# Kernel optimization log

Measured on AMD Instinct MI355X. Metric: run time of the kernel, lower is better.

Reference implementation:

```python
import jax, jax.numpy as jnp
import numpy as np
import math

DIM = 1024
NUM_HEADS = 16
HEAD_DIM = DIM // NUM_HEADS
ROPE_BASE = 10000.0


def _rope_cos_sin(seq_len, head_dim, dtype):
    inv_freq = 1.0 / (ROPE_BASE ** (jnp.arange(0, head_dim, 2, dtype=jnp.float32) / head_dim))
    t = jnp.arange(seq_len, dtype=jnp.float32)
    freqs = jnp.einsum('i,j->ij', t, inv_freq)          # (S, head_dim/2)
    emb = jnp.concatenate([freqs, freqs], axis=-1)      # (S, head_dim)
    return jnp.cos(emb).astype(dtype), jnp.sin(emb).astype(dtype)


def _rotate_half(x):
    x1, x2 = jnp.split(x, 2, axis=-1)
    return jnp.concatenate([-x2, x1], axis=-1)


def setup_inputs() -> dict:
    key = jax.random.key(0)
    kx, kq, kk, kv, ko = jax.random.split(key, 5)
    B, S = 4, 2048
    scale = 1.0 / math.sqrt(DIM)
    x = jax.random.normal(kx, (B, S, DIM), dtype=jnp.float32)
    Wq = jax.random.normal(kq, (DIM, DIM), dtype=jnp.float32) * scale
    Wk = jax.random.normal(kk, (DIM, DIM), dtype=jnp.float32) * scale
    Wv = jax.random.normal(kv, (DIM, DIM), dtype=jnp.float32) * scale
    Wo = jax.random.normal(ko, (DIM, DIM), dtype=jnp.float32) * scale
    mask = jnp.tril(jnp.ones((S, S), dtype=jnp.int32))  # causal mask
    return {"x": x, "Wq": Wq, "Wk": Wk, "Wv": Wv, "Wo": Wo, "mask": mask}


def reference(x, Wq, Wk, Wv, Wo, mask):
    B, S, _ = x.shape
    # projections (nn.Linear: y = x @ W.T)
    def split_heads(t):
        return t.reshape(B, S, NUM_HEADS, HEAD_DIM).transpose(0, 2, 1, 3)  # (B,H,S,D)
    q = split_heads(x @ Wq.T)
    k = split_heads(x @ Wk.T)
    v = split_heads(x @ Wv.T)
    # RoPE
    cos, sin = _rope_cos_sin(S, HEAD_DIM, x.dtype)      # (S, D)
    cos = cos[None, None]; sin = sin[None, None]
    q = q * cos + _rotate_half(q) * sin
    k = k * cos + _rotate_half(k) * sin
    # attention
    scores = jnp.einsum('bhsd,bhtd->bhst', q, k) / math.sqrt(HEAD_DIM)
    neg_inf = jnp.asarray(-jnp.inf, dtype=scores.dtype)
    scores = jnp.where(mask[None, None] == 0, neg_inf, scores)
    attn = jax.nn.softmax(scores, axis=-1)
    out = jnp.einsum('bhst,bhtd->bhsd', attn, v)        # (B,H,S,D)
    out = out.transpose(0, 2, 1, 3).reshape(B, S, DIM)
    return out @ Wo.T
```

## Files before the change

### kernel.cpp

```cpp
#include <hip/hip_runtime.h>
#include <hip/hip_bf16.h>

#define BDIM 1024
#define NH 16
#define HD 64
#define BB 4
#define SS 2048
#define MTOT (BB*SS)
#define NT (SS/64)

typedef __bf16 bf16x8 __attribute__((ext_vector_type(8)));
typedef float f32x4 __attribute__((ext_vector_type(4)));

__device__ __forceinline__ unsigned short f2b(float f){
    __bf16 h = (__bf16)f;
    return __builtin_bit_cast(unsigned short, h);
}

__device__ __forceinline__ unsigned cvtpk(float lo, float hi){
    unsigned u;
    asm("v_cvt_pk_bf16_f32 %0, %1, %2" : "=v"(u) : "v"(lo), "v"(hi));
    return u;
}

__device__ __forceinline__ void ld16(const unsigned short* g, unsigned short* l){
    __builtin_amdgcn_global_load_lds(
        (const __attribute__((address_space(1))) unsigned int*)(const void*)g,
        (__attribute__((address_space(3))) unsigned int*)(void*)l, 16, 0, 0);
}

__global__ void setup_all(const float* __restrict__ x,
                          const float* __restrict__ Wq, const float* __restrict__ Wk,
                          const float* __restrict__ Wv, const float* __restrict__ Wo,
                          unsigned short* __restrict__ xb,
                          unsigned short* __restrict__ oq, unsigned short* __restrict__ ok,
                          unsigned short* __restrict__ ov, unsigned short* __restrict__ oo,
                          float2* __restrict__ rt){
    const int bid = blockIdx.x;
    const int tid = threadIdx.x;
    if (bid < 8192){
        int i = bid * 256 + tid;
        float4 v = ((const float4*)x)[i];
        ushort4 o;
        o.x = f2b(v.x); o.y = f2b(v.y); o.z = f2b(v.z); o.w = f2b(v.w);
        ((ushort4*)xb)[i] = o;
    } else if (bid < 12288){
        int idx = bid - 8192;
        int which = idx >> 10;
        const float* in = (which == 0) ? Wq : (which == 1) ? Wk : (which == 2) ? Wv : Wo;
        unsigned short* out = (which == 0) ? oq : (which == 1) ? ok : (which == 2) ? ov : oo;
        int i = (idx & 1023) * 256 + tid;
        float4 v = ((const float4*)in)[i];
        ushort4 o;
        o.x = f2b(v.x); o.y = f2b(v.y); o.z = f2b(v.z); o.w = f2b(v.w);
        ((ushort4*)out)[i] = o;
    } else {
        int i = (bid - 12288) * 256 + tid;
        int s = i >> 5, d = i & 31;
        float theta = (float)s * exp2f(-0.41524101186092029f * (float)d);
        float sn, c;
        sincosf(theta, &sn, &c);
        rt[i] = make_float2(c, sn);
    }
}

#define TILE_US 4096

__device__ __forceinline__ void swz_xy(int& xs, int& ys){
    int id = blockIdx.x + 8*blockIdx.y;
    xs = id >> 6;
    int t = id & 63;
    ys = (t & 7)*8 + (t >> 3);
}

__device__ __forceinline__ void rope_store(
    const f32x4 acc[4][4], float qs, unsigned short* __restrict__ C,
    const float2* __restrict__ Rt, int m0, int bh, int wr, int lh, int ll)
{
    #pragma unroll
    for (int i = 0; i < 4; ++i)
        #pragma unroll
        for (int r = 0; r < 4; ++r){
            int m = m0 + wr*64 + i*16 + lh*4 + r;
            int s = m & (SS-1);
            int kt = s >> 6;
            const float2* rowcs = Rt + (s << 5);
            size_t fb = ((size_t)(bh*NT + kt)*8 + i)*512 + (size_t)(lh*4 + r)*8;
            #pragma unroll
            for (int jl = 0; jl < 2; ++jl){
                int d_lo = jl*16 + ll;
                float2 cs = rowcs[d_lo];
                float a_lo = acc[i][jl][r], a_hi = acc[i][jl+2][r];
                float y_lo = (a_lo*cs.x - a_hi*cs.y) * qs;
                float y_hi = (a_hi*cs.x + a_lo*cs.y) * qs;
                size_t off = fb + (size_t)(jl*2 + (ll>>3))*128 + (ll&7);
                C[off]        = f2b(y_lo);
                C[off + 2048] = f2b(y_hi);
            }
        }
}

__global__ __launch_bounds__(256, 2) void gemm_qkv(
    const unsigned short* __restrict__ Xb,
    const unsigned short* __restrict__ Wq,
    const unsigned short* __restrict__ Wk,
    const unsigned short* __restrict__ Wv,
    const float2* __restrict__ Rt,
    unsigned short* __restrict__ Qt,
    unsigned short* __restrict__ Kt,
    unsigned short* __restrict__ VTt)
{
    __shared__ alignas(16) unsigned short At [128*64];
    __shared__ alignas(16) unsigned short Bt0[128*64];
    __shared__ alignas(16) unsigned short Bt1[128*64];
    __shared__ alignas(16) unsigned short Bt2[128*64];

    int xs, ys;
    swz_xy(xs, ys);
    const int m0 = ys*128, n0 = xs*128;

    const int tid  = threadIdx.x;
    const int lane = tid & 63;
    const int wave = tid >> 6;
    const int wr = wave >> 1, wc = wave & 1;
    const int lh = lane >> 4, ll = lane & 15;
    const int K = 1024;

    f32x4 accq[4][4] = {}, acck[4][4] = {}, accv[4][4] = {};

    for (int k0 = 0; k0 < K; k0 += 64){
        #pragma unroll
        for (int c = 0; c < 4; ++c){
            int g   = c*256 + tid;
            int row = g >> 3;
            int off = (g & 7) * 8;
            int base = (c*256 + wave*64) * 8;
            ld16(Xb + (size_t)(m0+row)*K + k0 + off, At  + base);
            ld16(Wq + (size_t)(n0+row)*K + k0 + off, Bt0 + base);
            ld16(Wk + (size_t)(n0+row)*K + k0 + off, Bt1 + base);
            ld16(Wv + (size_t)(n0+row)*K + k0 + off, Bt2 + base);
        }
        __syncthreads();
        #pragma unroll
        for (int ks = 0; ks < 2; ++ks){
            bf16x8 af[4];
            #pragma unroll
            for (int i = 0; i < 4; ++i)
                af[i] = *(const bf16x8*)(At + (wr*64 + i*16 + ll)*64 + ks*32 + lh*8);
            {
                bf16x8 b[4];
                #pragma unroll
                for (int j = 0; j < 4; ++j)
                    b[j] = *(const bf16x8*)(Bt0 + (wc*64 + j*16 + ll)*64 + ks*32 + lh*8);
                #pragma unroll
                for (int i = 0; i < 4; ++i)
                    #pragma unroll
                    for (int j = 0; j < 4; ++j)
                        accq[i][j] = __builtin_amdgcn_mfma_f32_16x16x32_bf16(af[i], b[j], accq[i][j], 0, 0, 0);
            }
            {
                bf16x8 b[4];
                #pragma unroll
                for (int j = 0; j < 4; ++j)
                    b[j] = *(const bf16x8*)(Bt1 + (wc*64 + j*16 + ll)*64 + ks*32 + lh*8);
                #pragma unroll
                for (int i = 0; i < 4; ++i)
                    #pragma unroll
                    for (int j = 0; j < 4; ++j)
                        acck[i][j] = __builtin_amdgcn_mfma_f32_16x16x32_bf16(af[i], b[j], acck[i][j], 0, 0, 0);
            }
            {
                bf16x8 b[4];
                #pragma unroll
                for (int j = 0; j < 4; ++j)
                    b[j] = *(const bf16x8*)(Bt2 + (wc*64 + j*16 + ll)*64 + ks*32 + lh*8);
                #pragma unroll
                for (int i = 0; i < 4; ++i)
                    #pragma unroll
                    for (int j = 0; j < 4; ++j)
                        accv[i][j] = __builtin_amdgcn_mfma_f32_16x16x32_bf16(af[i], b[j], accv[i][j], 0, 0, 0);
            }
        }
        __syncthreads();
    }

    const int h  = xs*2 + wc;
    const int b  = m0 >> 11;
    const int bh = b*NH + h;

    rope_store(accq, 0.125f * 1.44269504f, Qt, Rt, m0, bh, wr, lh, ll);
    rope_store(acck, 1.0f,                 Kt, Rt, m0, bh, wr, lh, ll);

    {
        const int s0 = (m0 & (SS-1)) + wr*64;
        const int kt = s0 >> 6;
        #pragma unroll
        for (int i = 0; i < 4; ++i)
            #pragma unroll
            for (int j = 0; j < 4; ++j){
                unsigned short tmp[4];
                #pragma unroll
                for (int r = 0; r < 4; ++r)
                    tmp[r] = f2b(accv[i][j][r]);
                size_t off = ((size_t)(bh*NT + kt)*8 + (i>>1)*4 + j)*512
                           + (size_t)(((i&1)*2 + (lh>>1))*16 + ll)*8 + (lh&1)*4;
                *(uint2*)(VTt + off) = *(const uint2*)tmp;
            }
    }
}

__global__ __launch_bounds__(256, 4) void gemm_out(
    const unsigned short* __restrict__ Ab,
    const unsigned short* __restrict__ Wo,
    float* __restrict__ Cout)
{
    __shared__ alignas(16) unsigned short At[128*64];
    __shared__ alignas(16) unsigned short Bt[128*64];
    int xs, ys;
    swz_xy(xs, ys);
    const int m0 = ys * 128, n0 = xs * 128;

    const int tid  = threadIdx.x;
    const int lane = tid & 63;
    const int wave = tid >> 6;
    const int wr = wave >> 1, wc = wave & 1;
    const int lh = lane >> 4, ll = lane & 15;
    const int K = 1024;

    f32x4 acc[4][4] = {};
    for (int k0 = 0; k0 < K; k0 += 64){
        #pragma unroll
        for (int c = 0; c < 4; ++c){
            int g   = c*256 + tid;
            int row = g >> 3;
            int off = (g & 7) * 8;
            int base = (c*256 + wave*64) * 8;
            ld16(Ab + (size_t)(m0+row)*K + k0 + off, At + base);
            ld16(Wo + (size_t)(n0+row)*K + k0 + off, Bt + base);
        }
        __syncthreads();
        #pragma unroll
        for (int ks = 0; ks < 2; ++ks){
            bf16x8 af[4], bfr[4];
            #pragma unroll
            for (int i = 0; i < 4; ++i)
                af[i] = *(const bf16x8*)(At + (wr*64 + i*16 + ll)*64 + ks*32 + lh*8);
            #pragma unroll
            for (int j = 0; j < 4; ++j)
                bfr[j] = *(const bf16x8*)(Bt + (wc*64 + j*16 + ll)*64 + ks*32 + lh*8);
            #pragma unroll
            for (int i = 0; i < 4; ++i)
                #pragma unroll
                for (int j = 0; j < 4; ++j)
                    acc[i][j] = __builtin_amdgcn_mfma_f32_16x16x32_bf16(af[i], bfr[j], acc[i][j], 0, 0, 0);
        }
        __syncthreads();
    }

    #pragma unroll
    for (int i = 0; i < 4; ++i)
        #pragma unroll
        for (int j = 0; j < 4; ++j)
            #pragma unroll
            for (int r = 0; r < 4; ++r){
                int m = m0 + wr*64 + i*16 + lh*4 + r;
                int n = n0 + wc*64 + j*16 + ll;
                Cout[(size_t)m*BDIM + n] = acc[i][j][r];
            }
}

__device__ __forceinline__ void attn_tile(
    const bf16x8 qf[2], bool diag, int ws, int lane, int lh, int ll,
    const unsigned short* Ksh, const unsigned short* Vsh,
    float& li, f32x4 o[4])
{
    f32x4 sc[4] = {};
    #pragma unroll
    for (int ks = 0; ks < 2; ++ks)
        #pragma unroll
        for (int j = 0; j < 4; ++j){
            bf16x8 kfr = *(const bf16x8*)(Ksh + (ks*4 + j)*512 + lane*8);
            sc[j] = __builtin_amdgcn_mfma_f32_16x16x32_bf16(kfr, qf[ks], sc[j], 0, 0, 0);
        }
    if (diag){
        int qrow = ws*16 + ll;
        #pragma unroll
        for (int j = 0; j < 4; ++j)
            #pragma unroll
            for (int r = 0; r < 4; ++r)
                if (j*16 + lh*4 + r > qrow) sc[j][r] = -1e30f;
    }
    #pragma unroll
    for (int j = 0; j < 4; ++j)
        #pragma unroll
        for (int r = 0; r < 4; ++r)
            sc[j][r] = exp2f(sc[j][r] - 28.0f);
    float s = 0.f;
    #pragma unroll
    for (int j = 0; j < 4; ++j)
        s += (sc[j][0] + sc[j][1]) + (sc[j][2] + sc[j][3]);
    li += s;
    #pragma unroll
    for (int ks = 0; ks < 2; ++ks){
        unsigned a = cvtpk(sc[2*ks][0],   sc[2*ks][1]);
        unsigned b = cvtpk(sc[2*ks+1][0], sc[2*ks+1][1]);
        unsigned c = cvtpk(sc[2*ks][2],   sc[2*ks][3]);
        unsigned d = cvtpk(sc[2*ks+1][2], sc[2*ks+1][3]);
        asm("v_permlane32_swap_b32 %0, %1" : "+v"(a), "+v"(b));
        asm("v_permlane16_swap_b32 %0, %1" : "+v"(a), "+v"(b));
        asm("v_permlane32_swap_b32 %0, %1" : "+v"(c), "+v"(d));
        asm("v_permlane16_swap_b32 %0, %1" : "+v"(c), "+v"(d));
        uint4 uu = make_uint4(a, c, b, d);
        bf16x8 pf = __builtin_bit_cast(bf16x8, uu);
        #pragma unroll
        for (int t = 0; t < 4; ++t){
            bf16x8 vf = *(const bf16x8*)(Vsh + (ks*4 + t)*512 + lane*8);
            o[t] = __builtin_amdgcn_mfma_f32_16x16x32_bf16(pf, vf, o[t], 0, 0, 0);
        }
    }
}

__device__ __forceinline__ void store_o(
    unsigned short* S, const f32x4 o[4], const float li[4],
    int lane, int lh, int ll, int q0w, int b, int h,
    unsigned short* __restrict__ Obuf)
{
    #pragma unroll
    for (int r = 0; r < 4; ++r){
        float inv = 1.0f / li[r];
        #pragma unroll
        for (int t = 0; t < 4; ++t)
            S[(lh*4 + r)*72 + t*16 + ll] = f2b(o[t][r] * inv);
    }
    int row = lane >> 2, c4 = (lane & 3) * 8;
    size_t rb = ((size_t)(b*SS + q0w + row))*BDIM + h*HD;
    *(uint4*)(Obuf + rb + c4)      = *(uint4*)(S + row*72 + c4);
    *(uint4*)(Obuf + rb + 32 + c4) = *(uint4*)(S + row*72 + 32 + c4);
}

__global__ __launch_bounds__(512, 4) void attn_kernel(
    const unsigned short* __restrict__ Qt,
    const unsigned short* __restrict__ Kt,
    const unsigned short* __restrict__ VTt,
    unsigned short* __restrict__ Obuf)
{
    __shared__ alignas(16) unsigned short Ksh[2][TILE_US];
    __shared__ alignas(16) unsigned short Vsh[2][TILE_US];
    __shared__ alignas(16) unsigned short Psh[8][16*72];

    const int tid  = threadIdx.x;
    const int lane = tid & 63;
    const int wave = tid >> 6;
    const int grp  = wave >> 2;
    const int ws   = wave & 3;
    const int lh = lane >> 4, ll = lane & 15;
    const int bx = blockIdx.x;
    const int bh = blockIdx.y;

    const int tS = (grp == 0) ? bx        : 15 - bx;
    const int tL = (grp == 0) ? NT-1 - bx : 16 + bx;
    const int ktMax = NT-1 - bx;

    const unsigned short* Qhf = Qt  + (size_t)bh * NT * TILE_US;
    const unsigned short* Khf = Kt  + (size_t)bh * NT * TILE_US;
    const unsigned short* Vhf = VTt + (size_t)bh * NT * TILE_US;

    bf16x8 qfS[2], qfL[2];
    #pragma unroll
    for (int ks = 0; ks < 2; ++ks){
        qfS[ks] = *(const bf16x8*)(Qhf + (size_t)(tS*8 + ks*4 + ws)*512 + lane*8);
        qfL[ks] = *(const bf16x8*)(Qhf + (size_t)(tL*8 + ks*4 + ws)*512 + lane*8);
    }

    f32x4 oS[4] = {}, oL[4] = {};
    float liS = 0.f, liL = 0.f;

    const int tb = tid * 8;

    {
        uint4 k0 = *(const uint4*)(Khf + tb);
        uint4 v0 = *(const uint4*)(Vhf + tb);
        *(uint4*)(&Ksh[0][0] + tb) = k0;
        *(uint4*)(&Vsh[0][0] + tb) = v0;
    }
    __syncthreads();

    int cur = 0;
    for (int kt = 0; kt <= ktMax; ++kt){
        uint4 kr, vr;
        if (kt < ktMax){
            size_t nb = (size_t)(kt + 1) * TILE_US + tb;
            kr = *(const uint4*)(Khf + nb);
            vr = *(const uint4*)(Vhf + nb);
        }
        if (kt <= tL)
            attn_tile(qfL, kt == tL, ws, lane, lh, ll, &Ksh[cur][0], &Vsh[cur][0], liL, oL);
        if (kt <= tS)
            attn_tile(qfS, kt == tS, ws, lane, lh, ll, &Ksh[cur][0], &Vsh[cur][0], liS, oS);
        if (kt < ktMax){
            *(uint4*)(&Ksh[cur^1][0] + tb) = kr;
            *(uint4*)(&Vsh[cur^1][0] + tb) = vr;
        }
        __syncthreads();
        cur ^= 1;
    }

    liS += __shfl_xor(liS, 16); liS += __shfl_xor(liS, 32);
    liL += __shfl_xor(liL, 16); liL += __shfl_xor(liL, 32);
    float livS[4], livL[4];
    #pragma unroll
    for (int r = 0; r < 4; ++r){
        livS[r] = __shfl(liS, lh*4 + r);
        livL[r] = __shfl(liL, lh*4 + r);
    }

    int b = bh >> 4, h = bh & 15;
    store_o(Psh[wave], oS, livS, lane, lh, ll, tS*64 + ws*16, b, h, Obuf);
    store_o(Psh[wave], oL, livL, lane, lh, ll, tL*64 + ws*16, b, h, Obuf);
}

extern "C" void kernel_launch(void* const* d_in, const int* in_sizes, int n_in,
                              void* d_out, int out_size, void* d_ws, size_t ws_size,
                              hipStream_t stream) {
    const float* x  = (const float*)d_in[0];
    const float* Wq = (const float*)d_in[1];
    const float* Wk = (const float*)d_in[2];
    const float* Wv = (const float*)d_in[3];
    const float* Wo = (const float*)d_in[4];

    char* w = (char*)d_ws;
    unsigned short* xb  = (unsigned short*)(w);
    unsigned short* wqb = (unsigned short*)(w + (16u  << 20));
    unsigned short* wkb = (unsigned short*)(w + (18u  << 20));
    unsigned short* wvb = (unsigned short*)(w + (20u  << 20));
    unsigned short* wob = (unsigned short*)(w + (22u  << 20));
    unsigned short* Qt  = (unsigned short*)(w + (24u  << 20));
    unsigned short* Kt  = (unsigned short*)(w + (40u  << 20));
    unsigned short* VTt = (unsigned short*)(w + (56u  << 20));
    unsigned short* Ob  = (unsigned short*)(w + (72u  << 20));
    float2*         Rt  = (float2*)(w + (88u << 20));

    setup_all<<<12544, 256, 0, stream>>>(x, Wq, Wk, Wv, Wo, xb, wqb, wkb, wvb, wob, Rt);

    gemm_qkv<<<dim3(8, 64), 256, 0, stream>>>(xb, wqb, wkb, wvb, Rt, Qt, Kt, VTt);
    attn_kernel<<<dim3(8, 64), 512, 0, stream>>>(Qt, Kt, VTt, Ob);
    gemm_out<<<dim3(8, 64), 256, 0, stream>>>(Ob, wob, (float*)d_out);
}
```

Before: 292.9 us.

## Shrink QKV GEMM N-tile to one head and remap blocks per XCD

Halves the QKV projection tile width from 128 to 64 columns (one head per block), doubling the grid to 1024 blocks, shrinking shared memory and accumulators, and raising launch bounds to 3 blocks per CU. Each wave now covers 32 rows across all 64 columns, and the RoPE and V-transpose store indexing is updated to match. Block IDs are remapped so that consecutive IDs going to the same XCD share M rows, aiming at better L2 reuse of X. The cost is less operand reuse per block: each block loads the X tile for only half as much output.

```diff
diff --git a/kernel.cpp b/kernel.cpp
--- a/kernel.cpp
+++ b/kernel.cpp
@@ -73,34 +73,7 @@
     ys = (t & 7)*8 + (t >> 3);
 }
 
-__device__ __forceinline__ void rope_store(
-    const f32x4 acc[4][4], float qs, unsigned short* __restrict__ C,
-    const float2* __restrict__ Rt, int m0, int bh, int wr, int lh, int ll)
-{
-    #pragma unroll
-    for (int i = 0; i < 4; ++i)
-        #pragma unroll
-        for (int r = 0; r < 4; ++r){
-            int m = m0 + wr*64 + i*16 + lh*4 + r;
-            int s = m & (SS-1);
-            int kt = s >> 6;
-            const float2* rowcs = Rt + (s << 5);
-            size_t fb = ((size_t)(bh*NT + kt)*8 + i)*512 + (size_t)(lh*4 + r)*8;
-            #pragma unroll
-            for (int jl = 0; jl < 2; ++jl){
-                int d_lo = jl*16 + ll;
-                float2 cs = rowcs[d_lo];
-                float a_lo = acc[i][jl][r], a_hi = acc[i][jl+2][r];
-                float y_lo = (a_lo*cs.x - a_hi*cs.y) * qs;
-                float y_hi = (a_hi*cs.x + a_lo*cs.y) * qs;
-                size_t off = fb + (size_t)(jl*2 + (ll>>3))*128 + (ll&7);
-                C[off]        = f2b(y_lo);
-                C[off + 2048] = f2b(y_hi);
-            }
-        }
-}
-
-__global__ __launch_bounds__(256, 2) void gemm_qkv(
+__global__ __launch_bounds__(256, 3) void gemm_qkv(
     const unsigned short* __restrict__ Xb,
     const unsigned short* __restrict__ Wq,
     const unsigned short* __restrict__ Wk,
@@ -111,22 +84,25 @@
     unsigned short* __restrict__ VTt)
 {
     __shared__ alignas(16) unsigned short At [128*64];
-    __shared__ alignas(16) unsigned short Bt0[128*64];
-    __shared__ alignas(16) unsigned short Bt1[128*64];
-    __shared__ alignas(16) unsigned short Bt2[128*64];
-
-    int xs, ys;
-    swz_xy(xs, ys);
-    const int m0 = ys*128, n0 = xs*128;
+    __shared__ alignas(16) unsigned short Bt0[64*64];
+    __shared__ alignas(16) unsigned short Bt1[64*64];
+    __shared__ alignas(16) unsigned short Bt2[64*64];
+
+    const int id    = blockIdx.x + 16*blockIdx.y;
+    const int xcd   = id & 7;
+    const int chunk = id >> 3;
+    const int xs    = chunk >> 3;
+    const int ys    = xcd*8 + (chunk & 7);
+    const int m0 = ys*128, n0 = xs*64;
 
     const int tid  = threadIdx.x;
     const int lane = tid & 63;
     const int wave = tid >> 6;
-    const int wr = wave >> 1, wc = wave & 1;
+    const int wr   = wave;
     const int lh = lane >> 4, ll = lane & 15;
     const int K = 1024;
 
-    f32x4 accq[4][4] = {}, acck[4][4] = {}, accv[4][4] = {};
+    f32x4 accq[2][4] = {}, acck[2][4] = {}, accv[2][4] = {};
 
     for (int k0 = 0; k0 < K; k0 += 64){
         #pragma unroll
@@ -134,8 +110,14 @@
             int g   = c*256 + tid;
             int row = g >> 3;
             int off = (g & 7) * 8;
+            ld16(Xb + (size_t)(m0+row)*K + k0 + off, At + (c*256 + wave*64)*8);
+        }
+        #pragma unroll
+        for (int c = 0; c < 2; ++c){
+            int g   = c*256 + tid;
+            int row = g >> 3;
+            int off = (g & 7) * 8;
             int base = (c*256 + wave*64) * 8;
-            ld16(Xb + (size_t)(m0+row)*K + k0 + off, At  + base);
             ld16(Wq + (size_t)(n0+row)*K + k0 + off, Bt0 + base);
             ld16(Wk + (size_t)(n0+row)*K + k0 + off, Bt1 + base);
             ld16(Wv + (size_t)(n0+row)*K + k0 + off, Bt2 + base);
@@ -143,17 +125,17 @@
         __syncthreads();
         #pragma unroll
         for (int ks = 0; ks < 2; ++ks){
-            bf16x8 af[4];
-            #pragma unroll
-            for (int i = 0; i < 4; ++i)
-                af[i] = *(const bf16x8*)(At + (wr*64 + i*16 + ll)*64 + ks*32 + lh*8);
+            bf16x8 af[2];
+            #pragma unroll
+            for (int i = 0; i < 2; ++i)
+                af[i] = *(const bf16x8*)(At + (wr*32 + i*16 + ll)*64 + ks*32 + lh*8);
             {
                 bf16x8 b[4];
                 #pragma unroll
                 for (int j = 0; j < 4; ++j)
-                    b[j] = *(const bf16x8*)(Bt0 + (wc*64 + j*16 + ll)*64 + ks*32 + lh*8);
-                #pragma unroll
-                for (int i = 0; i < 4; ++i)
+                    b[j] = *(const bf16x8*)(Bt0 + (j*16 + ll)*64 + ks*32 + lh*8);
+                #pragma unroll
+                for (int i = 0; i < 2; ++i)
                     #pragma unroll
                     for (int j = 0; j < 4; ++j)
                         accq[i][j] = __builtin_amdgcn_mfma_f32_16x16x32_bf16(af[i], b[j], accq[i][j], 0, 0, 0);
@@ -162,9 +144,9 @@
                 bf16x8 b[4];
                 #pragma unroll
                 for (int j = 0; j < 4; ++j)
-                    b[j] = *(const bf16x8*)(Bt1 + (wc*64 + j*16 + ll)*64 + ks*32 + lh*8);
-                #pragma unroll
-                for (int i = 0; i < 4; ++i)
+                    b[j] = *(const bf16x8*)(Bt1 + (j*16 + ll)*64 + ks*32 + lh*8);
+                #pragma unroll
+                for (int i = 0; i < 2; ++i)
                     #pragma unroll
                     for (int j = 0; j < 4; ++j)
                         acck[i][j] = __builtin_amdgcn_mfma_f32_16x16x32_bf16(af[i], b[j], acck[i][j], 0, 0, 0);
@@ -173,9 +155,9 @@
                 bf16x8 b[4];
                 #pragma unroll
                 for (int j = 0; j < 4; ++j)
-                    b[j] = *(const bf16x8*)(Bt2 + (wc*64 + j*16 + ll)*64 + ks*32 + lh*8);
-                #pragma unroll
-                for (int i = 0; i < 4; ++i)
+                    b[j] = *(const bf16x8*)(Bt2 + (j*16 + ll)*64 + ks*32 + lh*8);
+                #pragma unroll
+                for (int i = 0; i < 2; ++i)
                     #pragma unroll
                     for (int j = 0; j < 4; ++j)
                         accv[i][j] = __builtin_amdgcn_mfma_f32_16x16x32_bf16(af[i], b[j], accv[i][j], 0, 0, 0);
@@ -184,28 +166,59 @@
         __syncthreads();
     }
 
-    const int h  = xs*2 + wc;
+    const int h  = xs;
     const int b  = m0 >> 11;
     const int bh = b*NH + h;
 
-    rope_store(accq, 0.125f * 1.44269504f, Qt, Rt, m0, bh, wr, lh, ll);
-    rope_store(acck, 1.0f,                 Kt, Rt, m0, bh, wr, lh, ll);
-
     {
-        const int s0 = (m0 & (SS-1)) + wr*64;
-        const int kt = s0 >> 6;
-        #pragma unroll
-        for (int i = 0; i < 4; ++i)
+        const float qsv[2] = {0.125f * 1.44269504f, 1.0f};
+        unsigned short* Cv[2] = {Qt, Kt};
+        #pragma unroll
+        for (int t2 = 0; t2 < 2; ++t2){
+            const f32x4 (*acc)[4] = (t2 == 0) ? accq : acck;
+            const float qs = qsv[t2];
+            unsigned short* C = Cv[t2];
+            #pragma unroll
+            for (int i = 0; i < 2; ++i)
+                #pragma unroll
+                for (int r = 0; r < 4; ++r){
+                    int m = m0 + wr*32 + i*16 + lh*4 + r;
+                    int s = m & (SS-1);
+                    int kt = s >> 6;
+                    int g = (wr*2 + i) & 3;
+                    const float2* rowcs = Rt + (s << 5);
+                    size_t fb = ((size_t)(bh*NT + kt)*8 + g)*512 + (size_t)(lh*4 + r)*8;
+                    #pragma unroll
+                    for (int jl = 0; jl < 2; ++jl){
+                        int d_lo = jl*16 + ll;
+                        float2 cs = rowcs[d_lo];
+                        float a_lo = acc[i][jl][r], a_hi = acc[i][jl+2][r];
+                        float y_lo = (a_lo*cs.x - a_hi*cs.y) * qs;
+                        float y_hi = (a_hi*cs.x + a_lo*cs.y) * qs;
+                        size_t off = fb + (size_t)(jl*2 + (ll>>3))*128 + (ll&7);
+                        C[off]        = f2b(y_lo);
+                        C[off + 2048] = f2b(y_hi);
+                    }
+                }
+        }
+    }
+
+    {
+        const int kt = ((m0 & (SS-1)) + wr*32) >> 6;
+        #pragma unroll
+        for (int i = 0; i < 2; ++i){
+            const int g = (wr*2 + i) & 3;
             #pragma unroll
             for (int j = 0; j < 4; ++j){
                 unsigned short tmp[4];
                 #pragma unroll
                 for (int r = 0; r < 4; ++r)
                     tmp[r] = f2b(accv[i][j][r]);
-                size_t off = ((size_t)(bh*NT + kt)*8 + (i>>1)*4 + j)*512
-                           + (size_t)(((i&1)*2 + (lh>>1))*16 + ll)*8 + (lh&1)*4;
+                size_t off = ((size_t)(bh*NT + kt)*8 + (g>>1)*4 + j)*512
+                           + (size_t)(((g&1)*2 + (lh>>1))*16 + ll)*8 + (lh&1)*4;
                 *(uint2*)(VTt + off) = *(const uint2*)tmp;
             }
+        }
     }
 }
 
@@ -442,7 +455,7 @@
 
     setup_all<<<12544, 256, 0, stream>>>(x, Wq, Wk, Wv, Wo, xb, wqb, wkb, wvb, wob, Rt);
 
-    gemm_qkv<<<dim3(8, 64), 256, 0, stream>>>(xb, wqb, wkb, wvb, Rt, Qt, Kt, VTt);
+    gemm_qkv<<<dim3(16, 64), 256, 0, stream>>>(xb, wqb, wkb, wvb, Rt, Qt, Kt, VTt);
     attn_kernel<<<dim3(8, 64), 512, 0, stream>>>(Qt, Kt, VTt, Ob);
     gemm_out<<<dim3(8, 64), 256, 0, stream>>>(Ob, wob, (float*)d_out);
 }
```

Measured after the change: 280.0 us. 1.05x faster.
